# Performance work log

Measured on AMD Instinct MI355X. Metric: run time of the kernel, lower is better.

## Reference

```python
import jax, jax.numpy as jnp
import numpy as np

STEPS = 2
P_TOPP = 0.9
TAU = 1.0
LN_EPS = 1e-5


def _top_p_attention(pooled, W1, W2, W3):
    # pooled: (N, C). Bilinear scores -> softmax -> nucleus (top-p) sparsify -> renorm.
    e1 = pooled @ W1.T                      # (N, d)
    e3 = pooled @ W3.T                      # (N, d)
    logits = (e1 @ W2.T) @ e3.T / TAU       # (N, N)
    attn = jax.nn.softmax(logits, axis=-1)
    srt = jnp.sort(attn, axis=-1)[:, ::-1]  # descending
    csum = jnp.cumsum(srt, axis=-1)
    keep = (csum - srt) < P_TOPP            # keep entries whose exclusive cum-prob < p
    thr = jnp.min(jnp.where(keep, srt, jnp.inf), axis=-1, keepdims=True)
    masked = jnp.where(attn >= thr, attn, 0.0)
    return masked / jnp.clip(jnp.sum(masked, axis=-1, keepdims=True), 1e-12)


def _layernorm(h, gamma, beta):
    mu = jnp.mean(h, axis=-1, keepdims=True)
    var = jnp.mean(jnp.square(h - mu), axis=-1, keepdims=True)
    return (h - mu) * jax.lax.rsqrt(var + LN_EPS) * gamma + beta


def _forward(x, prior, W1, W2, W3, prior_fwd_w, adaptive_w, ln_gamma, ln_beta, alpha):
    # Row-normalised prior (forward diffusion operator)
    Rf = prior / jnp.clip(jnp.sum(prior, axis=1, keepdims=True), 1e-12)
    Xf = x
    Xa = x
    residual = jnp.zeros_like(x)
    for idx in range(STEPS):
        pooled = jnp.mean(Xa, axis=1)                      # protein axis pooling -> (N_P, C)
        attn = _top_p_attention(pooled, W1, W2, W3)        # (N_P, N_P)
        Xf = jnp.einsum('ij,jkc->ikc', Rf, Xf)
        Xa = jnp.einsum('ij,jkc->ikc', attn, Xa)
        delta = jnp.einsum('ikc,dc->ikd', Xf, prior_fwd_w[idx]) \
              + jnp.einsum('ikc,dc->ikd', Xa, adaptive_w[idx])
        residual = residual + delta                        # dropout is identity in eval mode
    gate = jax.nn.sigmoid(alpha)                           # (1,)
    return _layernorm(x + gate * residual, ln_gamma, ln_beta)


def setup_inputs() -> dict:
    key = jax.random.key(0)
    ks = jax.random.split(key, 8)
    N_P, N_C, C, D = 2048, 64, 128, 64
    x = jax.random.normal(ks[0], (N_P, N_C, C), dtype=jnp.float32)
    prior = jax.random.uniform(ks[1], (N_P, N_P), dtype=jnp.float32)
    W1 = jax.random.normal(ks[2], (D, C), dtype=jnp.float32) / np.sqrt(C)
    W2 = jax.random.normal(ks[3], (D, D), dtype=jnp.float32) / np.sqrt(D)
    W3 = jax.random.normal(ks[4], (D, C), dtype=jnp.float32) / np.sqrt(C)
    prior_fwd_w = jax.random.normal(ks[5], (STEPS, C, C), dtype=jnp.float32) / np.sqrt(C)
    adaptive_w = jax.random.normal(ks[6], (STEPS, C, C), dtype=jnp.float32) / np.sqrt(C)
    ln_gamma = jnp.ones((C,), dtype=jnp.float32)
    ln_beta = jnp.zeros((C,), dtype=jnp.float32)
    alpha = jnp.zeros((1,), dtype=jnp.float32)
    return {"x": x, "prior": prior, "W1": W1, "W2": W2, "W3": W3,
            "prior_fwd_w": prior_fwd_w, "adaptive_w": adaptive_w,
            "ln_gamma": ln_gamma, "ln_beta": ln_beta, "alpha": alpha}


def reference(x, prior, W1, W2, W3, prior_fwd_w, adaptive_w, ln_gamma, ln_beta, alpha):
    return _forward(x, prior, W1, W2, W3, prior_fwd_w, adaptive_w, ln_gamma, ln_beta, alpha)
```

## Files before the change

### kernel.cpp

```cpp
#include <hip/hip_runtime.h>

typedef unsigned short u16;
typedef __attribute__((ext_vector_type(8))) short short8;
typedef __attribute__((ext_vector_type(4))) float f32x4;
typedef __attribute__((ext_vector_type(16))) float f32x16;

#define AS1 __attribute__((address_space(1)))
#define AS3 __attribute__((address_space(3)))

__device__ __forceinline__ void async_cp16(const void* g, void* l) {
  __builtin_amdgcn_global_load_lds((const AS1 unsigned int*)g, (AS3 unsigned int*)l, 16, 0, 0);
}

__device__ __forceinline__ u16 f2bf(float f) {
  union { float f; unsigned u; } v; v.f = f;
  unsigned r = v.u + 0x7fffu + ((v.u >> 16) & 1u);
  return (u16)(r >> 16);
}
__device__ __forceinline__ float bf2f(u16 h) {
  union { unsigned u; float f; } v; v.u = ((unsigned)h) << 16;
  return v.f;
}

template<int MODE>
__global__ __launch_bounds__(512, 2) void gemm32(
    const u16* __restrict__ A, const u16* __restrict__ B,
    int M, int N, int K,
    u16* __restrict__ Crow, int crow_ld, int crow_coloff,
    u16* __restrict__ Ct, int ct_ld)
{
  extern __shared__ u16 smem[];
  const int tid  = threadIdx.x;
  const int lane = tid & 63;
  const int w    = tid >> 6;
  const int m0 = blockIdx.y * 256;
  const int n0 = blockIdx.x * 256;
  const int wm = w >> 2;
  const int wn = w & 3;
  const int l31  = lane & 31;
  const int half = lane >> 5;
  const int pl   = (l31 & 3) ^ ((l31 >> 2) & 3);

  f32x16 acc[4][2];
#pragma unroll
  for (int i = 0; i < 4; i++)
#pragma unroll
    for (int j = 0; j < 2; j++)
#pragma unroll
      for (int r = 0; r < 16; r++) acc[i][j][r] = 0.f;

  const int sr4 = lane >> 2, sc4 = lane & 3;
  const int pp  = (sr4 & 3) ^ (sr4 >> 2);
  const int gko = (sc4 ^ pp) * 8;
  const u16* gA0 = A + (size_t)(m0 + w * 32 + sr4) * K + gko;
  const u16* gA1 = A + (size_t)(m0 + w * 32 + 16 + sr4) * K + gko;
  const u16* gB0 = B + (size_t)(n0 + w * 32 + sr4) * K + gko;
  const u16* gB1 = B + (size_t)(n0 + w * 32 + 16 + sr4) * K + gko;
  const int la = w * 1024;

#define ISSUE_A(tt) do {                                             \
    u16* sl = smem + ((tt) & 1) * 32768 + la;                        \
    const int ko = (tt) * 64;                                        \
    async_cp16(gA0 + ko, sl);           async_cp16(gA1 + ko, sl + 512);      \
    async_cp16(gA0 + ko + 32, sl + 8192); async_cp16(gA1 + ko + 32, sl + 8704);\
  } while (0)
#define ISSUE_B(tt) do {                                             \
    u16* sl = smem + ((tt) & 1) * 32768 + 16384 + la;                \
    const int ko = (tt) * 64;                                        \
    async_cp16(gB0 + ko, sl);           async_cp16(gB1 + ko, sl + 512);      \
    async_cp16(gB0 + ko + 32, sl + 8192); async_cp16(gB1 + ko + 32, sl + 8704);\
  } while (0)

  const int NT = K >> 6;
  ISSUE_A(0); ISSUE_B(0);
  asm volatile("s_waitcnt vmcnt(0)" ::: "memory");
  __builtin_amdgcn_s_barrier();

  for (int t = 0; t < NT; ++t) {
    const u16* sAp = smem + (t & 1) * 32768;
    const u16* sBp = sAp + 16384;
    const bool st = (t + 1 < NT);
    const int ar = (wm * 128 + l31) * 32;
    const int br = (wn * 64 + l31) * 32;
    short8 A01[2][4], A23[2][4], Bj0[4], Bj1[4];
#define FRAG_KC(ks) ((ks >> 1) * 8192 + ((((ks & 1) * 2 + half) ^ pl) * 8))

#pragma unroll
    for (int i = 0; i < 2; i++)
#pragma unroll
      for (int ks = 0; ks < 4; ks++)
        A01[i][ks] = *(const short8*)(sAp + ar + i * 1024 + FRAG_KC(ks));
#pragma unroll
    for (int ks = 0; ks < 4; ks++)
      Bj0[ks] = *(const short8*)(sBp + br + FRAG_KC(ks));
    if (st) ISSUE_A(t + 1);
    asm volatile("s_waitcnt lgkmcnt(8)" ::: "memory");
    __builtin_amdgcn_s_barrier();
    asm volatile("s_waitcnt lgkmcnt(0)" ::: "memory");
    __builtin_amdgcn_s_setprio(1);
#pragma unroll
    for (int i = 0; i < 2; i++)
#pragma unroll
      for (int ks = 0; ks < 4; ks++)
        acc[i][0] = __builtin_amdgcn_mfma_f32_32x32x16_bf16(A01[i][ks], Bj0[ks], acc[i][0], 0, 0, 0);
    __builtin_amdgcn_s_setprio(0);
    asm volatile("" ::: "memory");
    __builtin_amdgcn_s_barrier();

#pragma unroll
    for (int ks = 0; ks < 4; ks++)
      Bj1[ks] = *(const short8*)(sBp + br + 1024 + FRAG_KC(ks));
    if (st) ISSUE_B(t + 1);
    asm volatile("" ::: "memory");
    __builtin_amdgcn_s_barrier();
    asm volatile("s_waitcnt lgkmcnt(0)" ::: "memory");
    __builtin_amdgcn_s_setprio(1);
#pragma unroll
    for (int i = 0; i < 2; i++)
#pragma unroll
      for (int ks = 0; ks < 4; ks++)
        acc[i][1] = __builtin_amdgcn_mfma_f32_32x32x16_bf16(A01[i][ks], Bj1[ks], acc[i][1], 0, 0, 0);
    __builtin_amdgcn_s_setprio(0);
    asm volatile("" ::: "memory");
    __builtin_amdgcn_s_barrier();

#pragma unroll
    for (int i = 0; i < 2; i++)
#pragma unroll
      for (int ks = 0; ks < 4; ks++)
        A23[i][ks] = *(const short8*)(sAp + ar + 2048 + i * 1024 + FRAG_KC(ks));
    asm volatile("" ::: "memory");
    __builtin_amdgcn_s_barrier();
    asm volatile("s_waitcnt lgkmcnt(0)" ::: "memory");
    __builtin_amdgcn_s_setprio(1);
#pragma unroll
    for (int i = 0; i < 2; i++)
#pragma unroll
      for (int ks = 0; ks < 4; ks++)
        acc[2 + i][1] = __builtin_amdgcn_mfma_f32_32x32x16_bf16(A23[i][ks], Bj1[ks], acc[2 + i][1], 0, 0, 0);
    __builtin_amdgcn_s_setprio(0);
    asm volatile("" ::: "memory");
    __builtin_amdgcn_s_barrier();

    __builtin_amdgcn_s_setprio(1);
#pragma unroll
    for (int i = 0; i < 2; i++)
#pragma unroll
      for (int ks = 0; ks < 4; ks++)
        acc[2 + i][0] = __builtin_amdgcn_mfma_f32_32x32x16_bf16(A23[i][ks], Bj0[ks], acc[2 + i][0], 0, 0, 0);
    __builtin_amdgcn_s_setprio(0);
    asm volatile("s_waitcnt vmcnt(0)" ::: "memory");
    __builtin_amdgcn_s_barrier();
#undef FRAG_KC
  }
#undef ISSUE_A
#undef ISSUE_B

  u16* T = smem;

#pragma unroll
  for (int pr = 0; pr < 4; pr++) {
    if (wm == (pr >> 1)) {
#pragma unroll
      for (int ii = 0; ii < 2; ii++)
#pragma unroll
        for (int j = 0; j < 2; j++)
#pragma unroll
          for (int r = 0; r < 16; r++) {
            const int rloc = ii * 32 + (r & 3) + 8 * (r >> 2) + 4 * half;
            T[rloc * 264 + wn * 64 + j * 32 + l31] = f2bf(acc[(pr & 1) * 2 + ii][j][r]);
          }
    }
    __syncthreads();
    {
      const int row = tid >> 3, c8 = tid & 7;
      const size_t grow = (size_t)(m0 + pr * 64 + row);
      const size_t crow = grow * (size_t)(N >> 7) + (n0 >> 7) + (c8 >> 2);
      u16* dst = Crow + crow * (size_t)crow_ld + crow_coloff + (c8 & 3) * 32;
      const u16* src = T + row * 264 + c8 * 32;
#pragma unroll
      for (int u = 0; u < 4; u++) ((float4*)dst)[u] = ((const float4*)src)[u];
    }
    __syncthreads();
  }

  if constexpr (MODE == 1) {
#pragma unroll
    for (int p = 0; p < 4; p++) {
      if (wn == p) {
#pragma unroll
        for (int i = 0; i < 4; i++)
#pragma unroll
          for (int j = 0; j < 2; j++)
#pragma unroll
            for (int r = 0; r < 16; r++) {
              const int nloc = j * 32 + l31;
              const int mcol = wm * 128 + i * 32 + (r & 3) + 8 * (r >> 2) + 4 * half;
              T[nloc * 264 + mcol] = f2bf(acc[i][j][r]);
            }
      }
      __syncthreads();
      {
        const int row = tid >> 3, c8 = tid & 7;
        u16* dst = Ct + (size_t)(n0 + p * 64 + row) * ct_ld + m0 + c8 * 32;
        const u16* src = T + row * 264 + c8 * 32;
#pragma unroll
        for (int u = 0; u < 4; u++) ((float4*)dst)[u] = ((const float4*)src)[u];
      }
      __syncthreads();
    }
  }
}

template<int MODE>
__global__ __launch_bounds__(256) void gemm_bt(
    const u16* __restrict__ A, const u16* __restrict__ B,
    int M, int N, int K,
    float* __restrict__ Cf,
    u16* __restrict__ Crow, int crow_ld, int crow_coloff)
{
  extern __shared__ char smemc[];
  u16* sA = (u16*)smemc;
  u16* sB = (u16*)(smemc + 8192);
  const int tid  = threadIdx.x;
  const int lane = tid & 63;
  const int wid  = tid >> 6;
  const int m0 = blockIdx.y * 128;
  const int n0 = blockIdx.x * 128;
  const int wm = (wid >> 1) * 64;
  const int wn = (wid & 1) * 64;
  const int ml = lane & 15;
  const int qd = lane >> 4;

  f32x4 acc[4][4];
  const f32x4 zero = {0.f, 0.f, 0.f, 0.f};
#pragma unroll
  for (int i = 0; i < 4; i++)
#pragma unroll
    for (int j = 0; j < 4; j++) acc[i][j] = zero;

  const int r4 = tid >> 2;
  const int c4 = (tid & 3) * 8;
  const u16* gA0 = A + (size_t)(m0 + r4) * K + c4;
  const u16* gA1 = A + (size_t)(m0 + 64 + r4) * K + c4;
  const u16* gB0 = B + (size_t)(n0 + r4) * K + c4;
  const u16* gB1 = B + (size_t)(n0 + 64 + r4) * K + c4;
  u16* lA0 = sA + wid * 512;
  u16* lA1 = sA + 2048 + wid * 512;
  u16* lB0 = sB + wid * 512;
  u16* lB1 = sB + 2048 + wid * 512;

  for (int k0 = 0; k0 < K; k0 += 32) {
    async_cp16(gA0 + k0, lA0);
    async_cp16(gA1 + k0, lA1);
    async_cp16(gB0 + k0, lB0);
    async_cp16(gB1 + k0, lB1);
    __syncthreads();
    short8 af[4], bfr[4];
#pragma unroll
    for (int i = 0; i < 4; i++)
      af[i] = *(const short8*)(sA + (wm + i * 16 + ml) * 32 + qd * 8);
#pragma unroll
    for (int j = 0; j < 4; j++)
      bfr[j] = *(const short8*)(sB + (wn + j * 16 + ml) * 32 + qd * 8);
#pragma unroll
    for (int i = 0; i < 4; i++)
#pragma unroll
      for (int j = 0; j < 4; j++)
        acc[i][j] = __builtin_amdgcn_mfma_f32_16x16x32_bf16(af[i], bfr[j], acc[i][j], 0, 0, 0);
    __syncthreads();
  }

  if constexpr (MODE == 3) {
#pragma unroll
    for (int i = 0; i < 4; i++) {
      const int mr = m0 + wm + i * 16 + qd * 4;
#pragma unroll
      for (int j = 0; j < 4; j++) {
        const int nc = n0 + wn + j * 16 + ml;
        float* p = Cf + (size_t)mr * N + nc;
#pragma unroll
        for (int r = 0; r < 4; r++) p[(size_t)r * N] = acc[i][j][r];
      }
    }
  } else {
    u16* T = (u16*)smemc;
#pragma unroll
    for (int i = 0; i < 4; i++)
#pragma unroll
      for (int j = 0; j < 4; j++)
#pragma unroll
        for (int r = 0; r < 4; r++)
          T[(wm + i * 16 + qd * 4 + r) * 136 + wn + j * 16 + ml] = f2bf(acc[i][j][r]);
    __syncthreads();
    const int row = tid >> 1, halfr = tid & 1;
    const size_t crow = (size_t)(m0 + row) * (N >> 7) + (n0 >> 7);
    u16* dst = Crow + crow * (size_t)crow_ld + crow_coloff + halfr * 64;
    const u16* src = T + row * 136 + halfr * 64;
#pragma unroll
    for (int u = 0; u < 8; u++) ((float4*)dst)[u] = ((const float4*)src)[u];
  }
}

__global__ void rowsum_k(const float* __restrict__ prior, float* __restrict__ rs) {
  const int i = blockIdx.x, t = threadIdx.x;
  const float* p = prior + (size_t)i * 2048;
  float s = 0.f;
  for (int j = t; j < 2048; j += 256) s += p[j];
  __shared__ float red[256];
  red[t] = s; __syncthreads();
  for (int o = 128; o; o >>= 1) { if (t < o) red[t] += red[t + o]; __syncthreads(); }
  if (t == 0) rs[i] = red[0];
}

__global__ void convprior_k(const float4* __restrict__ prior, const float* __restrict__ rs,
                            ushort4* __restrict__ dst) {
  const int idx = blockIdx.x * 256 + threadIdx.x;
  const float inv = 1.0f / rs[idx >> 9];
  const float4 v = prior[idx];
  ushort4 o;
  o.x = f2bf(v.x * inv); o.y = f2bf(v.y * inv); o.z = f2bf(v.z * inv); o.w = f2bf(v.w * inv);
  dst[idx] = o;
}

__global__ void convx_k(const float* __restrict__ x, u16* __restrict__ xt) {
  __shared__ float S[64][65];
  const int t = threadIdx.x;
  const int j0 = blockIdx.y * 64;
  const int n0 = blockIdx.x * 64;
  const int rr = t >> 4, cxc = (t & 15) * 4;
#pragma unroll
  for (int p = 0; p < 4; p++) {
    const float4 v = *(const float4*)(x + (size_t)(j0 + rr + p * 16) * 8192 + n0 + cxc);
    S[rr + p * 16][cxc + 0] = v.x; S[rr + p * 16][cxc + 1] = v.y;
    S[rr + p * 16][cxc + 2] = v.z; S[rr + p * 16][cxc + 3] = v.w;
  }
  __syncthreads();
  const int nl = t >> 2, ch = (t & 3) * 16;
  alignas(16) u16 tmp[16];
#pragma unroll
  for (int u = 0; u < 16; u++) tmp[u] = f2bf(S[ch + u][nl]);
  float4* dst = (float4*)(xt + (size_t)(n0 + nl) * 2048 + j0 + ch);
  dst[0] = ((const float4*)tmp)[0];
  dst[1] = ((const float4*)tmp)[1];
}

__global__ void convw_k(const float* __restrict__ pw, const float* __restrict__ aw,
                        u16* __restrict__ btc) {
  const int idx = blockIdx.x * 256 + threadIdx.x;
  const int k = idx & 255, d = (idx >> 8) & 127, s = idx >> 15;
  const float v = (k < 128) ? aw[(s * 128 + d) * 128 + k] : pw[(s * 128 + d) * 128 + (k - 128)];
  btc[idx] = f2bf(v);
}

__global__ void pooled1_k(const float* __restrict__ x, float* __restrict__ pooled) {
  const int i = blockIdx.x, t = threadIdx.x;
  const int c = t & 127, h = t >> 7;
  const float* base = x + (size_t)i * 8192 + c;
  float s = 0.f;
  for (int k = h * 32; k < h * 32 + 32; k++) s += base[(size_t)k * 128];
  __shared__ float red[256];
  red[t] = s; __syncthreads();
  if (t < 128) pooled[i * 128 + t] = (red[t] + red[t + 128]) * (1.f / 64.f);
}

__global__ void pooled2_k(const u16* __restrict__ comb, float* __restrict__ pooled) {
  const int i = blockIdx.x, t = threadIdx.x;
  const int c = t & 127, h = t >> 7;
  const u16* base = comb + (size_t)i * 64 * 256 + c;
  float s = 0.f;
  for (int k = h * 32; k < h * 32 + 32; k++) s += bf2f(base[(size_t)k * 256]);
  __shared__ float red[256];
  red[t] = s; __syncthreads();
  if (t < 128) pooled[i * 128 + t] = (red[t] + red[t + 128]) * (1.f / 64.f);
}

__global__ void epre_k(const float* __restrict__ pooled,
                       const float* __restrict__ W1, const float* __restrict__ W2,
                       const float* __restrict__ W3,
                       u16* __restrict__ e3b, u16* __restrict__ fb) {
  const int i = blockIdx.x, d = threadIdx.x;
  __shared__ float pr[128], e1s[64];
  pr[d] = pooled[i * 128 + d];
  pr[d + 64] = pooled[i * 128 + 64 + d];
  __syncthreads();
  float s1 = 0.f, s3 = 0.f;
  for (int c = 0; c < 128; c++) {
    const float p = pr[c];
    s1 += p * W1[d * 128 + c];
    s3 += p * W3[d * 128 + c];
  }
  e1s[d] = s1;
  e3b[i * 64 + d] = f2bf(s3);
  __syncthreads();
  float sf = 0.f;
  for (int dd = 0; dd < 64; dd++) sf += e1s[dd] * W2[d * 64 + dd];
  fb[i * 64 + d] = f2bf(sf);
}

__device__ __forceinline__ float waveRedSum(float v) {
#pragma unroll
  for (int o = 1; o < 64; o <<= 1) v += __shfl_xor(v, o);
  return __shfl(v, 0);
}
__device__ __forceinline__ float waveRedMax(float v) {
#pragma unroll
  for (int o = 1; o < 64; o <<= 1) v = fmaxf(v, __shfl_xor(v, o));
  return __shfl(v, 0);
}

__global__ __launch_bounds__(256) void topp_k(const float* __restrict__ logits,
                                              u16* __restrict__ attnb) {
  const int w = threadIdx.x >> 6, l = threadIdx.x & 63;
  const int i = blockIdx.x * 4 + w;
  const float4* row = (const float4*)(logits + (size_t)i * 2048);
  float E[32];
  float mx = -1e30f;
#pragma unroll
  for (int k = 0; k < 8; k++) {
    const float4 v = row[k * 64 + l];
    E[k * 4 + 0] = v.x; E[k * 4 + 1] = v.y; E[k * 4 + 2] = v.z; E[k * 4 + 3] = v.w;
    mx = fmaxf(fmaxf(mx, fmaxf(v.x, v.y)), fmaxf(v.z, v.w));
  }
  mx = waveRedMax(mx);
  float S = 0.f;
#pragma unroll
  for (int u = 0; u < 32; u++) { E[u] = __expf(E[u] - mx); S += E[u]; }
  S = waveRedSum(S);
  const float target = 0.9f * S;
  float lo = 0.f, hi = 1.f;
  for (int it = 0; it < 32; ++it) {
    const float mid = 0.5f * (lo + hi);
    float g = 0.f;
#pragma unroll
    for (int u = 0; u < 32; u++) g += (E[u] > mid) ? E[u] : 0.f;
    g = waveRedSum(g);
    const bool below = (g < target);
    hi = below ? mid : hi;
    lo = below ? lo : mid;
  }
  float Sk = 0.f;
#pragma unroll
  for (int u = 0; u < 32; u++) Sk += (E[u] > lo) ? E[u] : 0.f;
  Sk = waveRedSum(Sk);
  const float inv = 1.f / Sk;
  u16* dst = attnb + (size_t)i * 2048;
#pragma unroll
  for (int k = 0; k < 8; k++) {
    ushort4 o;
    o.x = f2bf(E[k * 4 + 0] > lo ? E[k * 4 + 0] * inv : 0.f);
    o.y = f2bf(E[k * 4 + 1] > lo ? E[k * 4 + 1] * inv : 0.f);
    o.z = f2bf(E[k * 4 + 2] > lo ? E[k * 4 + 2] * inv : 0.f);
    o.w = f2bf(E[k * 4 + 3] > lo ? E[k * 4 + 3] * inv : 0.f);
    *(ushort4*)(dst + k * 256 + l * 4) = o;
  }
}

__global__ void ln_k(const float* __restrict__ x,
                     const u16* __restrict__ d1, const u16* __restrict__ d2,
                     float* __restrict__ out,
                     const float* __restrict__ gamma, const float* __restrict__ beta,
                     const float* __restrict__ alpha) {
  const int wid = threadIdx.x >> 6, lane = threadIdx.x & 63;
  const float gate = 1.f / (1.f + expf(-alpha[0]));
  const float2 g = ((const float2*)gamma)[lane];
  const float2 b = ((const float2*)beta)[lane];
#pragma unroll
  for (int rr = 0; rr < 2; ++rr) {
    const size_t row = (size_t)blockIdx.x * 8 + wid * 2 + rr;
    const float2 xv = ((const float2*)(x + row * 128))[lane];
    const ushort2 r1 = ((const ushort2*)(d1 + row * 128))[lane];
    const ushort2 r2 = ((const ushort2*)(d2 + row * 128))[lane];
    const float h0 = xv.x + gate * (bf2f(r1.x) + bf2f(r2.x));
    const float h1 = xv.y + gate * (bf2f(r1.y) + bf2f(r2.y));
    float s = h0 + h1;
#pragma unroll
    for (int o = 32; o; o >>= 1) s += __shfl_down(s, o);
    const float mu = __shfl(s, 0) * (1.f / 128.f);
    const float d0 = h0 - mu, dd1 = h1 - mu;
    float vs = d0 * d0 + dd1 * dd1;
#pragma unroll
    for (int o = 32; o; o >>= 1) vs += __shfl_down(vs, o);
    const float rstd = rsqrtf(__shfl(vs, 0) * (1.f / 128.f) + 1e-5f);
    float2* op = (float2*)(out + row * 128);
    float2 ov;
    ov.x = d0 * rstd * g.x + b.x;
    ov.y = dd1 * rstd * g.y + b.y;
    op[lane] = ov;
  }
}

extern "C" void kernel_launch(void* const* d_in, const int* in_sizes, int n_in,
                              void* d_out, int out_size, void* d_ws, size_t ws_size,
                              hipStream_t stream) {
  const float* x     = (const float*)d_in[0];
  const float* prior = (const float*)d_in[1];
  const float* W1    = (const float*)d_in[2];
  const float* W2    = (const float*)d_in[3];
  const float* W3    = (const float*)d_in[4];
  const float* Pw    = (const float*)d_in[5];
  const float* Aw    = (const float*)d_in[6];
  const float* gamma = (const float*)d_in[7];
  const float* beta  = (const float*)d_in[8];
  const float* alpha = (const float*)d_in[9];
  float* out = (float*)d_out;

  char* w = (char*)d_ws;
  u16*   Xt_x   = (u16*)(w);
  u16*   XtA    = (u16*)(w + 33554432);
  u16*   XtF    = (u16*)(w + 67108864);
  u16*   comb   = (u16*)(w + 100663296);
  u16*   priorS = (u16*)(w + 167772160);
  u16*   attnb  = (u16*)(w + 176160768);
  float* pooled = (float*)(w + 184549376);
  u16*   e3b    = (u16*)(w + 185597952);
  u16*   fb     = (u16*)(w + 186122240);
  float* rs     = (float*)(w + 186646528);
  u16*   btc    = (u16*)(w + 186654720);
  float* logits1 = (float*)(w + 33554432);
  float* logits2 = (float*)(w);
  u16*   d1      = (u16*)(w);
  u16*   d2      = (u16*)(w + 33554432);
  (void)in_sizes; (void)n_in; (void)ws_size;

  static bool attr_done = false;
  if (!attr_done) {
    hipFuncSetAttribute(reinterpret_cast<const void*>(gemm32<1>),
                        hipFuncAttributeMaxDynamicSharedMemorySize, 131072);
    hipFuncSetAttribute(reinterpret_cast<const void*>(gemm32<2>),
                        hipFuncAttributeMaxDynamicSharedMemorySize, 131072);
    attr_done = true;
  }

  rowsum_k   <<<2048, 256, 0, stream>>>(prior, rs);
  convprior_k<<<4096, 256, 0, stream>>>((const float4*)prior, rs, (ushort4*)priorS);
  convx_k    <<<dim3(128, 32), 256, 0, stream>>>(x, Xt_x);
  convw_k    <<<256, 256, 0, stream>>>(Pw, Aw, btc);

  pooled1_k  <<<2048, 256, 0, stream>>>(x, pooled);
  epre_k     <<<2048, 64, 0, stream>>>(pooled, W1, W2, W3, e3b, fb);
  gemm_bt<3> <<<dim3(16, 16), 256, 16384, stream>>>(fb, e3b, 2048, 2048, 64,
                                                    logits1, nullptr, 0, 0);
  topp_k     <<<512, 256, 0, stream>>>(logits1, attnb);

  gemm32<1><<<dim3(32, 8), 512, 131072, stream>>>(attnb,  Xt_x, 2048, 8192, 2048,
                                                  comb, 256, 0,   XtA, 2048);
  gemm32<1><<<dim3(32, 8), 512, 131072, stream>>>(priorS, Xt_x, 2048, 8192, 2048,
                                                  comb, 256, 128, XtF, 2048);

  pooled2_k  <<<2048, 256, 0, stream>>>(comb, pooled);
  epre_k     <<<2048, 64, 0, stream>>>(pooled, W1, W2, W3, e3b, fb);
  gemm_bt<3> <<<dim3(16, 16), 256, 16384, stream>>>(fb, e3b, 2048, 2048, 64,
                                                    logits2, nullptr, 0, 0);
  topp_k     <<<512, 256, 0, stream>>>(logits2, attnb);

  gemm_bt<2><<<dim3(1, 1024), 256, 34816, stream>>>(comb, btc, 131072, 128, 256,
                                                    nullptr, d1, 128, 0);

  gemm32<2><<<dim3(32, 8), 512, 131072, stream>>>(attnb,  XtA, 2048, 8192, 2048,
                                                  comb, 256, 0,   nullptr, 0);
  gemm32<2><<<dim3(32, 8), 512, 131072, stream>>>(priorS, XtF, 2048, 8192, 2048,
                                                  comb, 256, 128, nullptr, 0);

  gemm_bt<2><<<dim3(1, 1024), 256, 34816, stream>>>(comb, btc + 32768, 131072, 128, 256,
                                                    nullptr, d2, 128, 0);

  ln_k<<<16384, 256, 0, stream>>>(x, d1, d2, out, gamma, beta, alpha);
}
```

Measured before the change: 657.3 us.

## Switch GEMM mainloop to 4-stage K=32 async LDS pipeline with prefetch depth two

The bf16 MFMA GEMM mainloop moves from a double-buffered K=64 tile to a four-slot ring of K=32 tiles, issuing global-to-LDS copies two iterations ahead and waiting with vmcnt(4) instead of draining all loads. The four MFMA phases are merged into two per iteration, halving barriers per tile of K but doubling iteration count. The aim is to hide global load latency better; the cost is more loop iterations and barriers overall, with less MFMA work between synchronisations.

After: 663.1 us, median of 2. No clear change (+0.9%).

```diff
diff --git a/kernel.cpp b/kernel.cpp
--- a/kernel.cpp
+++ b/kernel.cpp
@@ -58,59 +58,66 @@
   const u16* gB1 = B + (size_t)(n0 + w * 32 + 16 + sr4) * K + gko;
   const int la = w * 1024;
 
-#define ISSUE_A(tt) do {                                             \
-    u16* sl = smem + ((tt) & 1) * 32768 + la;                        \
-    const int ko = (tt) * 64;                                        \
-    async_cp16(gA0 + ko, sl);           async_cp16(gA1 + ko, sl + 512);      \
-    async_cp16(gA0 + ko + 32, sl + 8192); async_cp16(gA1 + ko + 32, sl + 8704);\
+#define ISSUE_A(tt) do {                                   \
+    u16* sl = smem + ((tt) & 3) * 16384 + la;              \
+    const int ko = (tt) * 32;                              \
+    async_cp16(gA0 + ko, sl); async_cp16(gA1 + ko, sl + 512); \
   } while (0)
-#define ISSUE_B(tt) do {                                             \
-    u16* sl = smem + ((tt) & 1) * 32768 + 16384 + la;                \
-    const int ko = (tt) * 64;                                        \
-    async_cp16(gB0 + ko, sl);           async_cp16(gB1 + ko, sl + 512);      \
-    async_cp16(gB0 + ko + 32, sl + 8192); async_cp16(gB1 + ko + 32, sl + 8704);\
+#define ISSUE_B(tt) do {                                   \
+    u16* sl = smem + ((tt) & 3) * 16384 + 8192 + la;       \
+    const int ko = (tt) * 32;                              \
+    async_cp16(gB0 + ko, sl); async_cp16(gB1 + ko, sl + 512); \
   } while (0)
 
-  const int NT = K >> 6;
-  ISSUE_A(0); ISSUE_B(0);
-  asm volatile("s_waitcnt vmcnt(0)" ::: "memory");
+  const int NT = K >> 5;
+  ISSUE_A(0); ISSUE_B(0); ISSUE_A(1); ISSUE_B(1);
+  asm volatile("s_waitcnt vmcnt(4)" ::: "memory");
   __builtin_amdgcn_s_barrier();
 
   for (int t = 0; t < NT; ++t) {
-    const u16* sAp = smem + (t & 1) * 32768;
-    const u16* sBp = sAp + 16384;
-    const bool st = (t + 1 < NT);
+    const u16* sAp = smem + (t & 3) * 16384;
+    const u16* sBp = sAp + 8192;
+    const bool st = (t + 2 < NT);
     const int ar = (wm * 128 + l31) * 32;
     const int br = (wn * 64 + l31) * 32;
-    short8 A01[2][4], A23[2][4], Bj0[4], Bj1[4];
-#define FRAG_KC(ks) ((ks >> 1) * 8192 + ((((ks & 1) * 2 + half) ^ pl) * 8))
+    short8 A01[2][2], A23[2][2], Bj0[2], Bj1[2];
+#define FRAG(ks) ((((ks) * 2 + half) ^ pl) * 8)
 
 #pragma unroll
     for (int i = 0; i < 2; i++)
 #pragma unroll
-      for (int ks = 0; ks < 4; ks++)
-        A01[i][ks] = *(const short8*)(sAp + ar + i * 1024 + FRAG_KC(ks));
-#pragma unroll
-    for (int ks = 0; ks < 4; ks++)
-      Bj0[ks] = *(const short8*)(sBp + br + FRAG_KC(ks));
-    if (st) ISSUE_A(t + 1);
-    asm volatile("s_waitcnt lgkmcnt(8)" ::: "memory");
+      for (int ks = 0; ks < 2; ks++)
+        A01[i][ks] = *(const short8*)(sAp + ar + i * 1024 + FRAG(ks));
+#pragma unroll
+    for (int ks = 0; ks < 2; ks++) {
+      Bj0[ks] = *(const short8*)(sBp + br + FRAG(ks));
+      Bj1[ks] = *(const short8*)(sBp + br + 1024 + FRAG(ks));
+    }
+    if (st) ISSUE_A(t + 2);
+    asm volatile("s_waitcnt lgkmcnt(4)" ::: "memory");
     __builtin_amdgcn_s_barrier();
     asm volatile("s_waitcnt lgkmcnt(0)" ::: "memory");
     __builtin_amdgcn_s_setprio(1);
 #pragma unroll
     for (int i = 0; i < 2; i++)
 #pragma unroll
-      for (int ks = 0; ks < 4; ks++)
+      for (int ks = 0; ks < 2; ks++)
         acc[i][0] = __builtin_amdgcn_mfma_f32_32x32x16_bf16(A01[i][ks], Bj0[ks], acc[i][0], 0, 0, 0);
+#pragma unroll
+    for (int i = 0; i < 2; i++)
+#pragma unroll
+      for (int ks = 0; ks < 2; ks++)
+        acc[i][1] = __builtin_amdgcn_mfma_f32_32x32x16_bf16(A01[i][ks], Bj1[ks], acc[i][1], 0, 0, 0);
     __builtin_amdgcn_s_setprio(0);
     asm volatile("" ::: "memory");
     __builtin_amdgcn_s_barrier();
 
 #pragma unroll
-    for (int ks = 0; ks < 4; ks++)
-      Bj1[ks] = *(const short8*)(sBp + br + 1024 + FRAG_KC(ks));
-    if (st) ISSUE_B(t + 1);
+    for (int i = 0; i < 2; i++)
+#pragma unroll
+      for (int ks = 0; ks < 2; ks++)
+        A23[i][ks] = *(const short8*)(sAp + ar + 2048 + i * 1024 + FRAG(ks));
+    if (st) ISSUE_B(t + 2);
     asm volatile("" ::: "memory");
     __builtin_amdgcn_s_barrier();
     asm volatile("s_waitcnt lgkmcnt(0)" ::: "memory");
@@ -118,40 +125,18 @@
 #pragma unroll
     for (int i = 0; i < 2; i++)
 #pragma unroll
-      for (int ks = 0; ks < 4; ks++)
-        acc[i][1] = __builtin_amdgcn_mfma_f32_32x32x16_bf16(A01[i][ks], Bj1[ks], acc[i][1], 0, 0, 0);
-    __builtin_amdgcn_s_setprio(0);
-    asm volatile("" ::: "memory");
-    __builtin_amdgcn_s_barrier();
-
+      for (int ks = 0; ks < 2; ks++)
+        acc[2 + i][1] = __builtin_amdgcn_mfma_f32_32x32x16_bf16(A23[i][ks], Bj1[ks], acc[2 + i][1], 0, 0, 0);
 #pragma unroll
     for (int i = 0; i < 2; i++)
 #pragma unroll
-      for (int ks = 0; ks < 4; ks++)
-        A23[i][ks] = *(const short8*)(sAp + ar + 2048 + i * 1024 + FRAG_KC(ks));
-    asm volatile("" ::: "memory");
-    __builtin_amdgcn_s_barrier();
-    asm volatile("s_waitcnt lgkmcnt(0)" ::: "memory");
-    __builtin_amdgcn_s_setprio(1);
-#pragma unroll
-    for (int i = 0; i < 2; i++)
-#pragma unroll
-      for (int ks = 0; ks < 4; ks++)
-        acc[2 + i][1] = __builtin_amdgcn_mfma_f32_32x32x16_bf16(A23[i][ks], Bj1[ks], acc[2 + i][1], 0, 0, 0);
-    __builtin_amdgcn_s_setprio(0);
-    asm volatile("" ::: "memory");
-    __builtin_amdgcn_s_barrier();
-
-    __builtin_amdgcn_s_setprio(1);
-#pragma unroll
-    for (int i = 0; i < 2; i++)
-#pragma unroll
-      for (int ks = 0; ks < 4; ks++)
+      for (int ks = 0; ks < 2; ks++)
         acc[2 + i][0] = __builtin_amdgcn_mfma_f32_32x32x16_bf16(A23[i][ks], Bj0[ks], acc[2 + i][0], 0, 0, 0);
     __builtin_amdgcn_s_setprio(0);
-    asm volatile("s_waitcnt vmcnt(0)" ::: "memory");
+    if (st) { asm volatile("s_waitcnt vmcnt(4)" ::: "memory"); }
+    else    { asm volatile("s_waitcnt vmcnt(0)" ::: "memory"); }
     __builtin_amdgcn_s_barrier();
-#undef FRAG_KC
+#undef FRAG
   }
 #undef ISSUE_A
 #undef ISSUE_B
```
